# Kernel tuning notes

Hardware: AMD Instinct MI355X
Metric: run time of the kernel (lower is better)

## Reference

```python
import jax, jax.numpy as jnp
import numpy as np

N_NODES = 100000
N_EDGES = 1600000
D = 128


def _gine_layer(x, src, dst, e, W1, b1, W2, b2):
    # message: relu(x_j + e_ji), aggregate: sum at destination
    m = jax.nn.relu(x[src] + e)                       # [E, D]
    agg = jax.ops.segment_sum(m, dst, num_segments=x.shape[0])  # [N, D]
    h = agg + x                                       # (1 + eps) * x_i with eps = 0
    h = jax.nn.relu(jnp.dot(h, W1) + b1)
    return jnp.dot(h, W2) + b2


def setup_inputs() -> dict:
    key = jax.random.key(0)
    ks = jax.random.split(key, 16)
    s = 0.05
    inp = {
        "x": jax.random.normal(ks[0], (N_NODES, D), dtype=jnp.float32),
        "edge_index": jax.random.randint(ks[1], (2, N_EDGES), 0, N_NODES, dtype=jnp.int64) if jax.config.jax_enable_x64 else jax.random.randint(ks[1], (2, N_EDGES), 0, N_NODES, dtype=jnp.int32),
        "edge_attr": jax.random.randint(ks[2], (N_EDGES,), 0, 100, dtype=jnp.int32),
        "edge_emb": jax.random.normal(ks[3], (100, D), dtype=jnp.float32) * s,
        "Win": jax.random.normal(ks[4], (D, D), dtype=jnp.float32) * s,
        "b_in": jnp.zeros((D,), dtype=jnp.float32),
        "W1_0": jax.random.normal(ks[5], (D, D), dtype=jnp.float32) * s,
        "b1_0": jnp.zeros((D,), dtype=jnp.float32),
        "W2_0": jax.random.normal(ks[6], (D, D), dtype=jnp.float32) * s,
        "b2_0": jnp.zeros((D,), dtype=jnp.float32),
        "W1_1": jax.random.normal(ks[7], (D, D), dtype=jnp.float32) * s,
        "b1_1": jnp.zeros((D,), dtype=jnp.float32),
        "W2_1": jax.random.normal(ks[8], (D, D), dtype=jnp.float32) * s,
        "b2_1": jnp.zeros((D,), dtype=jnp.float32),
        "Wout": jax.random.normal(ks[9], (D, 1), dtype=jnp.float32) * s,
        "b_out": jnp.zeros((1,), dtype=jnp.float32),
    }
    return inp


def reference(x, edge_index, edge_attr, edge_emb, Win, b_in,
              W1_0, b1_0, W2_0, b2_0, W1_1, b1_1, W2_1, b2_1,
              Wout, b_out):
    src, dst = edge_index[0], edge_index[1]
    e = edge_emb[edge_attr]                 # [E, D] edge-attribute embedding lookup
    h = jnp.dot(x, Win) + b_in              # input_proj
    # layer 0: GINEConv + residual add + relu (norm=none, dropout off)
    h = jax.nn.relu(_gine_layer(h, src, dst, e, W1_0, b1_0, W2_0, b2_0) + h)
    # layer 1
    h = jax.nn.relu(_gine_layer(h, src, dst, e, W1_1, b1_1, W2_1, b2_1) + h)
    # output_mlp: single Linear(hidden, 1); no final activation, no pooling
    return jnp.dot(h, Wout) + b_out
```

## Files before the change

kernel.cpp:

```cpp
#include <hip/hip_runtime.h>

#define NN 100000
#define D 128
#define CHUNK 4096
#define BCSTRIDE 392
#define AGG_BLOCKS 1024

typedef __attribute__((ext_vector_type(8))) short short8;
typedef __attribute__((ext_vector_type(8))) unsigned short ushort8;
typedef __attribute__((ext_vector_type(4))) float f32x4;

__device__ __forceinline__ float4 ld4(const float* p) { return *(const float4*)p; }

__device__ __forceinline__ unsigned short f2bf(float f) {
    unsigned int u = __float_as_uint(f);
    unsigned int r = u + 0x7fffu + ((u >> 16) & 1u);
    return (unsigned short)(r >> 16);
}
__device__ __forceinline__ float bf2f(unsigned short h) {
    return __uint_as_float(((unsigned int)h) << 16);
}
__device__ __forceinline__ int swz(int rloc, int c) {
    return rloc * 128 + ((c + ((rloc >> 2) << 4)) & 127);
}

__global__ __launch_bounds__(256) void setup_all(
    const float* __restrict__ W0, const float* __restrict__ W1,
    const float* __restrict__ W2, const float* __restrict__ W3,
    const float* __restrict__ W4, unsigned short* __restrict__ wp,
    const float* __restrict__ emb, unsigned int* __restrict__ embp,
    int* __restrict__ binTotal)
{
    const int T = blockIdx.x * 256 + threadIdx.x;
    if (T < 5 * D * D) {
        const int w = T / (D * D);
        const int t = T % (D * D);
        const float* W = (w == 0) ? W0 : (w == 1) ? W1 : (w == 2) ? W2 : (w == 3) ? W3 : W4;
        const int j  = t & 7;
        const int L  = (t >> 3) & 63;
        const int ks = (t >> 9) & 3;
        const int nt = t >> 11;
        const float v = W[(ks * 32 + (L >> 4) * 8 + j) * D + nt * 16 + (L & 15)];
        const unsigned short h = f2bf(v);
        unsigned short* hi = wp + (size_t)w * 2 * D * D;
        hi[t] = h;
        hi[D * D + t] = f2bf(v - bf2f(h));
    } else if (T < 5 * D * D + 6400) {
        const int i = T - 5 * D * D;
        embp[i] = (unsigned int)f2bf(emb[i * 2]) | ((unsigned int)f2bf(emb[i * 2 + 1]) << 16);
    } else if (T < 5 * D * D + 6400 + BCSTRIDE) {
        binTotal[T - 5 * D * D - 6400] = 0;
    }
}

__global__ __launch_bounds__(256) void gemm_in(
    const float* __restrict__ A1,
    const unsigned short* __restrict__ Whi, const unsigned short* __restrict__ Wlo,
    const float* __restrict__ bias,
    unsigned short* __restrict__ out_hi, unsigned short* __restrict__ out_lo, int N)
{
    __shared__ __align__(16) unsigned int uT[64 * 128];
    const int t  = threadIdx.x;
    const int wv = t >> 6;
    const int L  = t & 63;
    const int lr = L & 15;
    const int q  = L >> 4;
    const int rbase = wv * 16;
    const int row = blockIdx.x * 64 + rbase + lr;

    short8 ahi[4], alo[4];
    #pragma unroll
    for (int ks = 0; ks < 4; ++ks) {
        float v[8];
        if (row < N) {
            const int off = row * D + ks * 32 + q * 8;
            const float4 x0 = ld4(&A1[off]), x1 = ld4(&A1[off + 4]);
            v[0] = x0.x; v[1] = x0.y; v[2] = x0.z; v[3] = x0.w;
            v[4] = x1.x; v[5] = x1.y; v[6] = x1.z; v[7] = x1.w;
        } else {
            #pragma unroll
            for (int j = 0; j < 8; ++j) v[j] = 0.f;
        }
        #pragma unroll
        for (int j = 0; j < 8; ++j) {
            const unsigned short h = f2bf(v[j]);
            ahi[ks][j] = (short)h;
            alo[ks][j] = (short)f2bf(v[j] - bf2f(h));
        }
    }

    f32x4 acc[8];
    #pragma unroll
    for (int nt = 0; nt < 8; ++nt) acc[nt] = (f32x4){0.f, 0.f, 0.f, 0.f};

    #pragma unroll
    for (int ks = 0; ks < 4; ++ks)
        #pragma unroll
        for (int nt = 0; nt < 8; ++nt) {
            const int base = ((nt * 4 + ks) * 64 + L) * 8;
            const short8 bhi = *(const short8*)&Whi[base];
            const short8 blo = *(const short8*)&Wlo[base];
            acc[nt] = __builtin_amdgcn_mfma_f32_16x16x32_bf16(alo[ks], bhi, acc[nt], 0, 0, 0);
            acc[nt] = __builtin_amdgcn_mfma_f32_16x16x32_bf16(ahi[ks], blo, acc[nt], 0, 0, 0);
            acc[nt] = __builtin_amdgcn_mfma_f32_16x16x32_bf16(ahi[ks], bhi, acc[nt], 0, 0, 0);
        }

    #pragma unroll
    for (int nt = 0; nt < 8; ++nt) {
        const float b = bias[nt * 16 + lr];
        #pragma unroll
        for (int r = 0; r < 4; ++r) {
            const int rloc = rbase + q * 4 + r;
            uT[swz(rloc, nt * 16 + lr)] = __float_as_uint(acc[nt][r] + b);
        }
    }
    __syncthreads();
    if (row < N) {
        const int rl = rbase + lr;
        #pragma unroll
        for (int ks = 0; ks < 4; ++ks) {
            const unsigned int* p = &uT[swz(rl, ks * 32 + q * 8)];
            const int off = row * D + ks * 32 + q * 8;
            ushort8 oh, ol;
            #pragma unroll
            for (int j = 0; j < 8; ++j) {
                const float o = __uint_as_float(p[j]);
                const unsigned short h = f2bf(o);
                oh[j] = h;
                ol[j] = f2bf(o - bf2f(h));
            }
            *(ushort8*)&out_hi[off] = oh;
            *(ushort8*)&out_lo[off] = ol;
        }
    }
}

template<bool LAST>
__global__ __launch_bounds__(256) void mlp_fused(
    const float* __restrict__ agg,
    const unsigned short* __restrict__ h_hi, const unsigned short* __restrict__ h_lo,
    const unsigned short* __restrict__ W1hi, const unsigned short* __restrict__ W1lo,
    const float* __restrict__ b1,
    const unsigned short* __restrict__ W2hi, const unsigned short* __restrict__ W2lo,
    const float* __restrict__ b2,
    unsigned short* __restrict__ out_hi, unsigned short* __restrict__ out_lo,
    const float* __restrict__ Wout, const float* __restrict__ bout,
    float* __restrict__ outv, int N)
{
    __shared__ __align__(16) unsigned int uT[64 * 128];
    const int t  = threadIdx.x;
    const int wv = t >> 6;
    const int L  = t & 63;
    const int lr = L & 15;
    const int q  = L >> 4;
    const int rbase = wv * 16;
    const int row = blockIdx.x * 64 + rbase + lr;
    const int rl = rbase + lr;

    ushort8 hh[4], ll[4];
    short8 ahi[4], alo[4];
    #pragma unroll
    for (int ks = 0; ks < 4; ++ks) {
        float v[8];
        if (row < N) {
            const int off = row * D + ks * 32 + q * 8;
            const float4 x0 = ld4(&agg[off]), x1 = ld4(&agg[off + 4]);
            hh[ks] = *(const ushort8*)&h_hi[off];
            ll[ks] = *(const ushort8*)&h_lo[off];
            v[0] = x0.x; v[1] = x0.y; v[2] = x0.z; v[3] = x0.w;
            v[4] = x1.x; v[5] = x1.y; v[6] = x1.z; v[7] = x1.w;
        } else {
            hh[ks] = (ushort8)0; ll[ks] = (ushort8)0;
            #pragma unroll
            for (int j = 0; j < 8; ++j) v[j] = 0.f;
        }
        #pragma unroll
        for (int j = 0; j < 8; ++j) {
            v[j] += bf2f(hh[ks][j]) + bf2f(ll[ks][j]);
            const unsigned short h = f2bf(v[j]);
            ahi[ks][j] = (short)h;
            alo[ks][j] = (short)f2bf(v[j] - bf2f(h));
        }
    }

    f32x4 acc[8];
    #pragma unroll
    for (int nt = 0; nt < 8; ++nt) acc[nt] = (f32x4){0.f, 0.f, 0.f, 0.f};

    #pragma unroll
    for (int ks = 0; ks < 4; ++ks)
        #pragma unroll
        for (int nt = 0; nt < 8; ++nt) {
            const int base = ((nt * 4 + ks) * 64 + L) * 8;
            const short8 bhi = *(const short8*)&W1hi[base];
            const short8 blo = *(const short8*)&W1lo[base];
            acc[nt] = __builtin_amdgcn_mfma_f32_16x16x32_bf16(alo[ks], bhi, acc[nt], 0, 0, 0);
            acc[nt] = __builtin_amdgcn_mfma_f32_16x16x32_bf16(ahi[ks], blo, acc[nt], 0, 0, 0);
            acc[nt] = __builtin_amdgcn_mfma_f32_16x16x32_bf16(ahi[ks], bhi, acc[nt], 0, 0, 0);
        }

    #pragma unroll
    for (int nt = 0; nt < 8; ++nt) {
        const float b = b1[nt * 16 + lr];
        #pragma unroll
        for (int r = 0; r < 4; ++r) {
            const int rloc = rbase + q * 4 + r;
            const float o = fmaxf(acc[nt][r] + b, 0.f);
            const unsigned int hi = f2bf(o);
            const unsigned int lo = f2bf(o - bf2f((unsigned short)hi));
            uT[swz(rloc, nt * 16 + lr)] = (hi << 16) | lo;
        }
    }
    __syncthreads();

    short8 uhi[4], ulo[4];
    #pragma unroll
    for (int ks = 0; ks < 4; ++ks) {
        const unsigned int* p = &uT[swz(rl, ks * 32 + q * 8)];
        #pragma unroll
        for (int j = 0; j < 8; ++j) {
            const unsigned int v = p[j];
            uhi[ks][j] = (short)(v >> 16);
            ulo[ks][j] = (short)(v & 0xffffu);
        }
    }

    f32x4 acc2[8];
    #pragma unroll
    for (int nt = 0; nt < 8; ++nt) acc2[nt] = (f32x4){0.f, 0.f, 0.f, 0.f};

    #pragma unroll
    for (int ks = 0; ks < 4; ++ks)
        #pragma unroll
        for (int nt = 0; nt < 8; ++nt) {
            const int base = ((nt * 4 + ks) * 64 + L) * 8;
            const short8 bhi = *(const short8*)&W2hi[base];
            const short8 blo = *(const short8*)&W2lo[base];
            acc2[nt] = __builtin_amdgcn_mfma_f32_16x16x32_bf16(ulo[ks], bhi, acc2[nt], 0, 0, 0);
            acc2[nt] = __builtin_amdgcn_mfma_f32_16x16x32_bf16(uhi[ks], blo, acc2[nt], 0, 0, 0);
            acc2[nt] = __builtin_amdgcn_mfma_f32_16x16x32_bf16(uhi[ks], bhi, acc2[nt], 0, 0, 0);
        }
    __syncthreads();

    #pragma unroll
    for (int nt = 0; nt < 8; ++nt) {
        const float b = b2[nt * 16 + lr];
        #pragma unroll
        for (int r = 0; r < 4; ++r) {
            const int rloc = rbase + q * 4 + r;
            uT[swz(rloc, nt * 16 + lr)] = __float_as_uint(acc2[nt][r] + b);
        }
    }
    __syncthreads();

    if (LAST) {
        float accv = 0.f;
        if (row < N) {
            #pragma unroll
            for (int ks = 0; ks < 4; ++ks) {
                const unsigned int* p = &uT[swz(rl, ks * 32 + q * 8)];
                const float4 w0 = ld4(&Wout[ks * 32 + q * 8]);
                const float4 w1 = ld4(&Wout[ks * 32 + q * 8 + 4]);
                float o[8];
                #pragma unroll
                for (int j = 0; j < 8; ++j)
                    o[j] = fmaxf(__uint_as_float(p[j]) + bf2f(hh[ks][j]) + bf2f(ll[ks][j]), 0.f);
                accv += o[0] * w0.x + o[1] * w0.y + o[2] * w0.z + o[3] * w0.w;
                accv += o[4] * w1.x + o[5] * w1.y + o[6] * w1.z + o[7] * w1.w;
            }
        }
        accv += __shfl_xor(accv, 16);
        accv += __shfl_xor(accv, 32);
        if (q == 0 && row < N) outv[row] = accv + bout[0];
    } else if (row < N) {
        #pragma unroll
        for (int ks = 0; ks < 4; ++ks) {
            const unsigned int* p = &uT[swz(rl, ks * 32 + q * 8)];
            const int off = row * D + ks * 32 + q * 8;
            ushort8 oh, ol;
            #pragma unroll
            for (int j = 0; j < 8; ++j) {
                const float o = fmaxf(__uint_as_float(p[j]) + bf2f(hh[ks][j]) + bf2f(ll[ks][j]), 0.f);
                const unsigned short h = f2bf(o);
                oh[j] = h;
                ol[j] = f2bf(o - bf2f(h));
            }
            *(ushort8*)&out_hi[off] = oh;
            *(ushort8*)&out_lo[off] = ol;
        }
    }
}

__global__ __launch_bounds__(256) void bin_count(
    const int* __restrict__ dst, int* __restrict__ blkcnt,
    int* __restrict__ binTotal, int E, int nbins)
{
    __shared__ int hist[512];
    const int t = threadIdx.x;
    const int i = blockIdx.x;
    for (int k = t; k < nbins; k += 256) hist[k] = 0;
    __syncthreads();
    const int e0 = i * CHUNK;
    const int e1 = min(E, e0 + CHUNK);
    for (int e = e0 + t; e < e1; e += 256) atomicAdd(&hist[dst[e] >> 8], 1);
    __syncthreads();
    for (int k = t; k < nbins; k += 256) {
        const int c = hist[k];
        blkcnt[i * BCSTRIDE + k] = c;
        if (c) atomicAdd(&binTotal[k], c);
    }
}

__global__ __launch_bounds__(512) void bin_scan(
    const int* __restrict__ binTotal, int* __restrict__ binStart,
    int* __restrict__ binCursor, int nbins)
{
    __shared__ int s[512];
    const int t = threadIdx.x;
    const int v = (t < nbins) ? binTotal[t] : 0;
    s[t] = v;
    __syncthreads();
    for (int off = 1; off < 512; off <<= 1) {
        const int x = (t >= off) ? s[t - off] : 0;
        __syncthreads();
        s[t] += x;
        __syncthreads();
    }
    if (t < nbins) { binStart[t] = s[t] - v; binCursor[t] = s[t] - v; }
    if (t == 0)    binStart[nbins] = s[511];
}

__global__ __launch_bounds__(256) void bin_scatter(
    const int* __restrict__ src, const int* __restrict__ dst,
    const int* __restrict__ attr, const int* __restrict__ blkcnt,
    int* __restrict__ binCursor, int2* __restrict__ binned, int E, int nbins)
{
    __shared__ int cur[512];
    const int t = threadIdx.x;
    const int i = blockIdx.x;
    for (int k = t; k < nbins; k += 256) {
        const int c = blkcnt[i * BCSTRIDE + k];
        if (c) cur[k] = atomicAdd(&binCursor[k], c);
    }
    __syncthreads();
    const int e0 = i * CHUNK;
    const int e1 = min(E, e0 + CHUNK);
    for (int e = e0 + t; e < e1; e += 256) {
        const int d = dst[e];
        const int p = atomicAdd(&cur[d >> 8], 1);
        binned[p] = make_int2(src[e] | (attr[e] << 20), d);
    }
}

__global__ __launch_bounds__(256) void bin_build(
    const int2* __restrict__ binned, const int* __restrict__ binStart,
    int* __restrict__ rowptr, int* __restrict__ epack, int N)
{
    __shared__ int hist[256];
    __shared__ int scn[256];
    __shared__ int curn[256];
    const int t = threadIdx.x;
    const int b = blockIdx.x;
    hist[t] = 0;
    __syncthreads();
    const int ebeg = binStart[b];
    const int eend = binStart[b + 1];
    for (int e = ebeg + t; e < eend; e += 256) atomicAdd(&hist[binned[e].y & 255], 1);
    __syncthreads();
    scn[t] = hist[t];
    __syncthreads();
    for (int off = 1; off < 256; off <<= 1) {
        const int x = (t >= off) ? scn[t - off] : 0;
        __syncthreads();
        scn[t] += x;
        __syncthreads();
    }
    const int node = b * 256 + t;
    if (node < N) rowptr[node] = ebeg + scn[t];
    curn[t] = ebeg + scn[t] - hist[t];
    __syncthreads();
    for (int e = ebeg + t; e < eend; e += 256) {
        const int2 v = binned[e];
        const int p = atomicAdd(&curn[v.y & 255], 1);
        epack[p] = v.x;
    }
}

__global__ __launch_bounds__(512) void aggregate(
    const unsigned int* __restrict__ hu,
    const int* __restrict__ rowptr, const int* __restrict__ epack,
    const unsigned int* __restrict__ embp, float* __restrict__ agg, int N)
{
    __shared__ unsigned int semb[100 * 64];
    const int t = threadIdx.x;
    for (int i = t; i < 100 * 64; i += 512) semb[i] = embp[i];
    __syncthreads();

    const int wv   = t >> 6;
    const int lane = t & 63;

    for (int node = blockIdx.x * 8 + wv; node < N; node += AGG_BLOCKS * 8) {
        int start = (node == 0) ? 0 : rowptr[node - 1];
        int end   = rowptr[node];
        start = __builtin_amdgcn_readfirstlane(start);
        end   = __builtin_amdgcn_readfirstlane(end);

        float ax = 0.f, ay = 0.f;
        int j = start;

        for (; j < end && (j & 3); ++j) {
            const int p0 = __builtin_amdgcn_readfirstlane(epack[j]);
            const unsigned int u0 = hu[(p0 & 0xFFFFF) * 64 + lane];
            const unsigned int v0 = semb[(p0 >> 20) * 64 + lane];
            ax += fmaxf(__uint_as_float(u0 << 16) + __uint_as_float(v0 << 16), 0.f);
            ay += fmaxf(__uint_as_float(u0 & 0xffff0000u) + __uint_as_float(v0 & 0xffff0000u), 0.f);
        }

        for (; j + 7 < end; j += 8) {
            const int4 pk0 = *(const int4*)&epack[j];
            const int4 pk1 = *(const int4*)&epack[j + 4];
            int p[8];
            p[0] = __builtin_amdgcn_readfirstlane(pk0.x);
            p[1] = __builtin_amdgcn_readfirstlane(pk0.y);
            p[2] = __builtin_amdgcn_readfirstlane(pk0.z);
            p[3] = __builtin_amdgcn_readfirstlane(pk0.w);
            p[4] = __builtin_amdgcn_readfirstlane(pk1.x);
            p[5] = __builtin_amdgcn_readfirstlane(pk1.y);
            p[6] = __builtin_amdgcn_readfirstlane(pk1.z);
            p[7] = __builtin_amdgcn_readfirstlane(pk1.w);
            unsigned int u[8], v[8];
            #pragma unroll
            for (int k = 0; k < 8; ++k) u[k] = hu[(p[k] & 0xFFFFF) * 64 + lane];
            #pragma unroll
            for (int k = 0; k < 8; ++k) v[k] = semb[(p[k] >> 20) * 64 + lane];
            #pragma unroll
            for (int k = 0; k < 8; ++k) {
                ax += fmaxf(__uint_as_float(u[k] << 16) + __uint_as_float(v[k] << 16), 0.f);
                ay += fmaxf(__uint_as_float(u[k] & 0xffff0000u) + __uint_as_float(v[k] & 0xffff0000u), 0.f);
            }
        }

        if (j + 3 < end) {
            const int4 pk0 = *(const int4*)&epack[j];
            int p[4];
            p[0] = __builtin_amdgcn_readfirstlane(pk0.x);
            p[1] = __builtin_amdgcn_readfirstlane(pk0.y);
            p[2] = __builtin_amdgcn_readfirstlane(pk0.z);
            p[3] = __builtin_amdgcn_readfirstlane(pk0.w);
            unsigned int u[4], v[4];
            #pragma unroll
            for (int k = 0; k < 4; ++k) u[k] = hu[(p[k] & 0xFFFFF) * 64 + lane];
            #pragma unroll
            for (int k = 0; k < 4; ++k) v[k] = semb[(p[k] >> 20) * 64 + lane];
            #pragma unroll
            for (int k = 0; k < 4; ++k) {
                ax += fmaxf(__uint_as_float(u[k] << 16) + __uint_as_float(v[k] << 16), 0.f);
                ay += fmaxf(__uint_as_float(u[k] & 0xffff0000u) + __uint_as_float(v[k] & 0xffff0000u), 0.f);
            }
            j += 4;
        }

        for (; j < end; ++j) {
            const int p0 = __builtin_amdgcn_readfirstlane(epack[j]);
            const unsigned int u0 = hu[(p0 & 0xFFFFF) * 64 + lane];
            const unsigned int v0 = semb[(p0 >> 20) * 64 + lane];
            ax += fmaxf(__uint_as_float(u0 << 16) + __uint_as_float(v0 << 16), 0.f);
            ay += fmaxf(__uint_as_float(u0 & 0xffff0000u) + __uint_as_float(v0 & 0xffff0000u), 0.f);
        }

        float2 o; o.x = ax; o.y = ay;
        ((float2*)agg)[node * 64 + lane] = o;
    }
}

extern "C" void kernel_launch(void* const* d_in, const int* in_sizes, int n_in,
                              void* d_out, int out_size, void* d_ws, size_t ws_size,
                              hipStream_t stream)
{
    const float* x     = (const float*)d_in[0];
    const int*   ei    = (const int*)  d_in[1];
    const int*   attr  = (const int*)  d_in[2];
    const float* emb   = (const float*)d_in[3];
    const float* Win   = (const float*)d_in[4];
    const float* b_in  = (const float*)d_in[5];
    const float* W1_0  = (const float*)d_in[6];
    const float* b1_0  = (const float*)d_in[7];
    const float* W2_0  = (const float*)d_in[8];
    const float* b2_0  = (const float*)d_in[9];
    const float* W1_1  = (const float*)d_in[10];
    const float* b1_1  = (const float*)d_in[11];
    const float* W2_1  = (const float*)d_in[12];
    const float* b2_1  = (const float*)d_in[13];
    const float* Wout  = (const float*)d_in[14];
    const float* b_out = (const float*)d_in[15];
    float* out = (float*)d_out;

    const int N = NN;
    const int E = in_sizes[2];
    const int* srcp = ei;
    const int* dstp = ei + E;
    const int nbins = (N + 255) >> 8;
    const int eblocks = (E + CHUNK - 1) / CHUNK;

    unsigned short* h_hi = (unsigned short*)d_ws;
    unsigned short* h_lo = h_hi + (size_t)N * D;
    float* agg    = (float*)(h_lo + (size_t)N * D);
    int*   rowptr = (int*)(agg + (size_t)N * D);
    int*   epack  = rowptr + N;
    unsigned short* wp = (unsigned short*)(epack + E);
    unsigned short* Whi[5], *Wlo[5];
    for (int i = 0; i < 5; ++i) {
        Whi[i] = wp + (size_t)i * 2 * D * D;
        Wlo[i] = Whi[i] + D * D;
    }
    unsigned int* embp = (unsigned int*)(wp + 5 * 2 * D * D);
    int2* binned    = (int2*)agg;
    int*  blkcnt    = (int*)(binned + E);
    int*  binTotal  = blkcnt + eblocks * BCSTRIDE;
    int*  binStart  = binTotal + BCSTRIDE;
    int*  binCursor = binStart + BCSTRIDE;

    dim3 blk(256);
    const int fgrid = (N + 63) / 64;
    const int sgrid = (5 * D * D + 6400 + BCSTRIDE + 255) / 256;

    setup_all<<<sgrid, blk, 0, stream>>>(Win, W1_0, W2_0, W1_1, W2_1, wp, emb, embp, binTotal);

    bin_count<<<eblocks, blk, 0, stream>>>(dstp, blkcnt, binTotal, E, nbins);
    bin_scan<<<1, 512, 0, stream>>>(binTotal, binStart, binCursor, nbins);
    bin_scatter<<<eblocks, blk, 0, stream>>>(srcp, dstp, attr, blkcnt, binCursor, binned, E, nbins);
    bin_build<<<nbins, blk, 0, stream>>>(binned, binStart, rowptr, epack, N);

    gemm_in<<<fgrid, blk, 0, stream>>>(x, Whi[0], Wlo[0], b_in, h_hi, h_lo, N);

    aggregate<<<AGG_BLOCKS, dim3(512), 0, stream>>>(
        (const unsigned int*)h_hi, rowptr, epack, embp, agg, N);
    mlp_fused<false><<<fgrid, blk, 0, stream>>>(
        agg, h_hi, h_lo, Whi[1], Wlo[1], b1_0, Whi[2], Wlo[2], b2_0,
        h_hi, h_lo, nullptr, nullptr, nullptr, N);

    aggregate<<<AGG_BLOCKS, dim3(512), 0, stream>>>(
        (const unsigned int*)h_hi, rowptr, epack, embp, agg, N);
    mlp_fused<true><<<fgrid, blk, 0, stream>>>(
        agg, h_hi, h_lo, Whi[3], Wlo[3], b1_1, Whi[4], Wlo[4], b2_1,
        nullptr, nullptr, Wout, b_out, out, N);
}
```

Baseline: 458.4 us.

## Process two 16-row groups per wave to reuse weight fragments in GEMM kernels

gemm_in and mlp_fused now give each wave 32 rows as two 16-row MFMA groups, so blocks cover 128 rows and the grid is halved. Each hi/lo weight fragment loaded from global memory now feeds MFMAs for both groups, which halves weight-load traffic per row. To offset the extra accumulator registers, the residual h_hi/h_lo values are reloaded from global memory in the epilogue instead of being held in registers. The same LDS staging buffer is reused for both groups one after the other. This raises register pressure and may lower occupancy, and it adds a second read of the residual activations.

```diff
diff --git a/kernel.cpp b/kernel.cpp
--- a/kernel.cpp
+++ b/kernel.cpp
@@ -66,32 +66,40 @@
     const int lr = L & 15;
     const int q  = L >> 4;
     const int rbase = wv * 16;
-    const int row = blockIdx.x * 64 + rbase + lr;
-
-    short8 ahi[4], alo[4];
-    #pragma unroll
-    for (int ks = 0; ks < 4; ++ks) {
-        float v[8];
-        if (row < N) {
-            const int off = row * D + ks * 32 + q * 8;
-            const float4 x0 = ld4(&A1[off]), x1 = ld4(&A1[off + 4]);
-            v[0] = x0.x; v[1] = x0.y; v[2] = x0.z; v[3] = x0.w;
-            v[4] = x1.x; v[5] = x1.y; v[6] = x1.z; v[7] = x1.w;
-        } else {
-            #pragma unroll
-            for (int j = 0; j < 8; ++j) v[j] = 0.f;
-        }
-        #pragma unroll
-        for (int j = 0; j < 8; ++j) {
-            const unsigned short h = f2bf(v[j]);
-            ahi[ks][j] = (short)h;
-            alo[ks][j] = (short)f2bf(v[j] - bf2f(h));
-        }
-    }
-
-    f32x4 acc[8];
-    #pragma unroll
-    for (int nt = 0; nt < 8; ++nt) acc[nt] = (f32x4){0.f, 0.f, 0.f, 0.f};
+    const int row0 = blockIdx.x * 128 + wv * 32 + lr;
+    const int rl = rbase + lr;
+
+    short8 ahi[2][4], alo[2][4];
+    #pragma unroll
+    for (int g = 0; g < 2; ++g) {
+        const int row = row0 + g * 16;
+        #pragma unroll
+        for (int ks = 0; ks < 4; ++ks) {
+            float v[8];
+            if (row < N) {
+                const int off = row * D + ks * 32 + q * 8;
+                const float4 x0 = ld4(&A1[off]), x1 = ld4(&A1[off + 4]);
+                v[0] = x0.x; v[1] = x0.y; v[2] = x0.z; v[3] = x0.w;
+                v[4] = x1.x; v[5] = x1.y; v[6] = x1.z; v[7] = x1.w;
+            } else {
+                #pragma unroll
+                for (int j = 0; j < 8; ++j) v[j] = 0.f;
+            }
+            #pragma unroll
+            for (int j = 0; j < 8; ++j) {
+                const unsigned short h = f2bf(v[j]);
+                ahi[g][ks][j] = (short)h;
+                alo[g][ks][j] = (short)f2bf(v[j] - bf2f(h));
+            }
+        }
+    }
+    __syncthreads();
+
+    f32x4 acc[2][8];
+    #pragma unroll
+    for (int g = 0; g < 2; ++g)
+        #pragma unroll
+        for (int nt = 0; nt < 8; ++nt) acc[g][nt] = (f32x4){0.f, 0.f, 0.f, 0.f};
 
     #pragma unroll
     for (int ks = 0; ks < 4; ++ks)
@@ -100,37 +108,43 @@
             const int base = ((nt * 4 + ks) * 64 + L) * 8;
             const short8 bhi = *(const short8*)&Whi[base];
             const short8 blo = *(const short8*)&Wlo[base];
-            acc[nt] = __builtin_amdgcn_mfma_f32_16x16x32_bf16(alo[ks], bhi, acc[nt], 0, 0, 0);
-            acc[nt] = __builtin_amdgcn_mfma_f32_16x16x32_bf16(ahi[ks], blo, acc[nt], 0, 0, 0);
-            acc[nt] = __builtin_amdgcn_mfma_f32_16x16x32_bf16(ahi[ks], bhi, acc[nt], 0, 0, 0);
-        }
-
-    #pragma unroll
-    for (int nt = 0; nt < 8; ++nt) {
-        const float b = bias[nt * 16 + lr];
-        #pragma unroll
-        for (int r = 0; r < 4; ++r) {
-            const int rloc = rbase + q * 4 + r;
-            uT[swz(rloc, nt * 16 + lr)] = __float_as_uint(acc[nt][r] + b);
-        }
-    }
-    __syncthreads();
-    if (row < N) {
-        const int rl = rbase + lr;
-        #pragma unroll
-        for (int ks = 0; ks < 4; ++ks) {
-            const unsigned int* p = &uT[swz(rl, ks * 32 + q * 8)];
-            const int off = row * D + ks * 32 + q * 8;
-            ushort8 oh, ol;
-            #pragma unroll
-            for (int j = 0; j < 8; ++j) {
-                const float o = __uint_as_float(p[j]);
-                const unsigned short h = f2bf(o);
-                oh[j] = h;
-                ol[j] = f2bf(o - bf2f(h));
-            }
-            *(ushort8*)&out_hi[off] = oh;
-            *(ushort8*)&out_lo[off] = ol;
+            acc[0][nt] = __builtin_amdgcn_mfma_f32_16x16x32_bf16(alo[0][ks], bhi, acc[0][nt], 0, 0, 0);
+            acc[0][nt] = __builtin_amdgcn_mfma_f32_16x16x32_bf16(ahi[0][ks], blo, acc[0][nt], 0, 0, 0);
+            acc[0][nt] = __builtin_amdgcn_mfma_f32_16x16x32_bf16(ahi[0][ks], bhi, acc[0][nt], 0, 0, 0);
+            acc[1][nt] = __builtin_amdgcn_mfma_f32_16x16x32_bf16(alo[1][ks], bhi, acc[1][nt], 0, 0, 0);
+            acc[1][nt] = __builtin_amdgcn_mfma_f32_16x16x32_bf16(ahi[1][ks], blo, acc[1][nt], 0, 0, 0);
+            acc[1][nt] = __builtin_amdgcn_mfma_f32_16x16x32_bf16(ahi[1][ks], bhi, acc[1][nt], 0, 0, 0);
+        }
+    __syncthreads();
+
+    #pragma unroll
+    for (int g = 0; g < 2; ++g) {
+        const int row = row0 + g * 16;
+        #pragma unroll
+        for (int nt = 0; nt < 8; ++nt) {
+            const float b = bias[nt * 16 + lr];
+            #pragma unroll
+            for (int r = 0; r < 4; ++r) {
+                const int rloc = rbase + q * 4 + r;
+                uT[swz(rloc, nt * 16 + lr)] = __float_as_uint(acc[g][nt][r] + b);
+            }
+        }
+        if (row < N) {
+            #pragma unroll
+            for (int ks = 0; ks < 4; ++ks) {
+                const unsigned int* p = &uT[swz(rl, ks * 32 + q * 8)];
+                const int off = row * D + ks * 32 + q * 8;
+                ushort8 oh, ol;
+                #pragma unroll
+                for (int j = 0; j < 8; ++j) {
+                    const float o = __uint_as_float(p[j]);
+                    const unsigned short h = f2bf(o);
+                    oh[j] = h;
+                    ol[j] = f2bf(o - bf2f(h));
+                }
+                *(ushort8*)&out_hi[off] = oh;
+                *(ushort8*)&out_lo[off] = ol;
+            }
         }
     }
 }
@@ -138,12 +152,12 @@
 template<bool LAST>
 __global__ __launch_bounds__(256) void mlp_fused(
     const float* __restrict__ agg,
-    const unsigned short* __restrict__ h_hi, const unsigned short* __restrict__ h_lo,
+    const unsigned short* h_hi, const unsigned short* h_lo,
     const unsigned short* __restrict__ W1hi, const unsigned short* __restrict__ W1lo,
     const float* __restrict__ b1,
     const unsigned short* __restrict__ W2hi, const unsigned short* __restrict__ W2lo,
     const float* __restrict__ b2,
-    unsigned short* __restrict__ out_hi, unsigned short* __restrict__ out_lo,
+    unsigned short* out_hi, unsigned short* out_lo,
     const float* __restrict__ Wout, const float* __restrict__ bout,
     float* __restrict__ outv, int N)
 {
@@ -154,38 +168,44 @@
     const int lr = L & 15;
     const int q  = L >> 4;
     const int rbase = wv * 16;
-    const int row = blockIdx.x * 64 + rbase + lr;
+    const int row0 = blockIdx.x * 128 + wv * 32 + lr;
     const int rl = rbase + lr;
 
-    ushort8 hh[4], ll[4];
-    short8 ahi[4], alo[4];
-    #pragma unroll
-    for (int ks = 0; ks < 4; ++ks) {
-        float v[8];
-        if (row < N) {
-            const int off = row * D + ks * 32 + q * 8;
-            const float4 x0 = ld4(&agg[off]), x1 = ld4(&agg[off + 4]);
-            hh[ks] = *(const ushort8*)&h_hi[off];
-            ll[ks] = *(const ushort8*)&h_lo[off];
-            v[0] = x0.x; v[1] = x0.y; v[2] = x0.z; v[3] = x0.w;
-            v[4] = x1.x; v[5] = x1.y; v[6] = x1.z; v[7] = x1.w;
-        } else {
-            hh[ks] = (ushort8)0; ll[ks] = (ushort8)0;
-            #pragma unroll
-            for (int j = 0; j < 8; ++j) v[j] = 0.f;
-        }
-        #pragma unroll
-        for (int j = 0; j < 8; ++j) {
-            v[j] += bf2f(hh[ks][j]) + bf2f(ll[ks][j]);
-            const unsigned short h = f2bf(v[j]);
-            ahi[ks][j] = (short)h;
-            alo[ks][j] = (short)f2bf(v[j] - bf2f(h));
-        }
-    }
-
-    f32x4 acc[8];
-    #pragma unroll
-    for (int nt = 0; nt < 8; ++nt) acc[nt] = (f32x4){0.f, 0.f, 0.f, 0.f};
+    short8 ahi[2][4], alo[2][4];
+    #pragma unroll
+    for (int g = 0; g < 2; ++g) {
+        const int row = row0 + g * 16;
+        #pragma unroll
+        for (int ks = 0; ks < 4; ++ks) {
+            float v[8];
+            if (row < N) {
+                const int off = row * D + ks * 32 + q * 8;
+                const float4 x0 = ld4(&agg[off]), x1 = ld4(&agg[off + 4]);
+                const ushort8 hh = *(const ushort8*)&h_hi[off];
+                const ushort8 ll = *(const ushort8*)&h_lo[off];
+                v[0] = x0.x; v[1] = x0.y; v[2] = x0.z; v[3] = x0.w;
+                v[4] = x1.x; v[5] = x1.y; v[6] = x1.z; v[7] = x1.w;
+                #pragma unroll
+                for (int j = 0; j < 8; ++j) v[j] += bf2f(hh[j]) + bf2f(ll[j]);
+            } else {
+                #pragma unroll
+                for (int j = 0; j < 8; ++j) v[j] = 0.f;
+            }
+            #pragma unroll
+            for (int j = 0; j < 8; ++j) {
+                const unsigned short h = f2bf(v[j]);
+                ahi[g][ks][j] = (short)h;
+                alo[g][ks][j] = (short)f2bf(v[j] - bf2f(h));
+            }
+        }
+    }
+    __syncthreads();
+
+    f32x4 acc[2][8];
+    #pragma unroll
+    for (int g = 0; g < 2; ++g)
+        #pragma unroll
+        for (int nt = 0; nt < 8; ++nt) acc[g][nt] = (f32x4){0.f, 0.f, 0.f, 0.f};
 
     #pragma unroll
     for (int ks = 0; ks < 4; ++ks)
@@ -194,40 +214,48 @@
             const int base = ((nt * 4 + ks) * 64 + L) * 8;
             const short8 bhi = *(const short8*)&W1hi[base];
             const short8 blo = *(const short8*)&W1lo[base];
-            acc[nt] = __builtin_amdgcn_mfma_f32_16x16x32_bf16(alo[ks], bhi, acc[nt], 0, 0, 0);
-            acc[nt] = __builtin_amdgcn_mfma_f32_16x16x32_bf16(ahi[ks], blo, acc[nt], 0, 0, 0);
-            acc[nt] = __builtin_amdgcn_mfma_f32_16x16x32_bf16(ahi[ks], bhi, acc[nt], 0, 0, 0);
-        }
-
-    #pragma unroll
-    for (int nt = 0; nt < 8; ++nt) {
-        const float b = b1[nt * 16 + lr];
-        #pragma unroll
-        for (int r = 0; r < 4; ++r) {
-            const int rloc = rbase + q * 4 + r;
-            const float o = fmaxf(acc[nt][r] + b, 0.f);
-            const unsigned int hi = f2bf(o);
-            const unsigned int lo = f2bf(o - bf2f((unsigned short)hi));
-            uT[swz(rloc, nt * 16 + lr)] = (hi << 16) | lo;
-        }
-    }
-    __syncthreads();
-
-    short8 uhi[4], ulo[4];
-    #pragma unroll
-    for (int ks = 0; ks < 4; ++ks) {
-        const unsigned int* p = &uT[swz(rl, ks * 32 + q * 8)];
-        #pragma unroll
-        for (int j = 0; j < 8; ++j) {
-            const unsigned int v = p[j];
-            uhi[ks][j] = (short)(v >> 16);
-            ulo[ks][j] = (short)(v & 0xffffu);
-        }
-    }
-
-    f32x4 acc2[8];
-    #pragma unroll
-    for (int nt = 0; nt < 8; ++nt) acc2[nt] = (f32x4){0.f, 0.f, 0.f, 0.f};
+            acc[0][nt] = __builtin_amdgcn_mfma_f32_16x16x32_bf16(alo[0][ks], bhi, acc[0][nt], 0, 0, 0);
+            acc[0][nt] = __builtin_amdgcn_mfma_f32_16x16x32_bf16(ahi[0][ks], blo, acc[0][nt], 0, 0, 0);
+            acc[0][nt] = __builtin_amdgcn_mfma_f32_16x16x32_bf16(ahi[0][ks], bhi, acc[0][nt], 0, 0, 0);
+            acc[1][nt] = __builtin_amdgcn_mfma_f32_16x16x32_bf16(alo[1][ks], bhi, acc[1][nt], 0, 0, 0);
+            acc[1][nt] = __builtin_amdgcn_mfma_f32_16x16x32_bf16(ahi[1][ks], blo, acc[1][nt], 0, 0, 0);
+            acc[1][nt] = __builtin_amdgcn_mfma_f32_16x16x32_bf16(ahi[1][ks], bhi, acc[1][nt], 0, 0, 0);
+        }
+    __syncthreads();
+
+    short8 uhi[2][4], ulo[2][4];
+    #pragma unroll
+    for (int g = 0; g < 2; ++g) {
+        #pragma unroll
+        for (int nt = 0; nt < 8; ++nt) {
+            const float b = b1[nt * 16 + lr];
+            #pragma unroll
+            for (int r = 0; r < 4; ++r) {
+                const int rloc = rbase + q * 4 + r;
+                const float o = fmaxf(acc[g][nt][r] + b, 0.f);
+                const unsigned int hi = f2bf(o);
+                const unsigned int lo = f2bf(o - bf2f((unsigned short)hi));
+                uT[swz(rloc, nt * 16 + lr)] = (hi << 16) | lo;
+            }
+        }
+        #pragma unroll
+        for (int ks = 0; ks < 4; ++ks) {
+            const unsigned int* p = &uT[swz(rl, ks * 32 + q * 8)];
+            #pragma unroll
+            for (int j = 0; j < 8; ++j) {
+                const unsigned int v = p[j];
+                uhi[g][ks][j] = (short)(v >> 16);
+                ulo[g][ks][j] = (short)(v & 0xffffu);
+            }
+        }
+    }
+    __syncthreads();
+
+    f32x4 acc2[2][8];
+    #pragma unroll
+    for (int g = 0; g < 2; ++g)
+        #pragma unroll
+        for (int nt = 0; nt < 8; ++nt) acc2[g][nt] = (f32x4){0.f, 0.f, 0.f, 0.f};
 
     #pragma unroll
     for (int ks = 0; ks < 4; ++ks)
@@ -236,57 +264,67 @@
             const int base = ((nt * 4 + ks) * 64 + L) * 8;
             const short8 bhi = *(const short8*)&W2hi[base];
             const short8 blo = *(const short8*)&W2lo[base];
-            acc2[nt] = __builtin_amdgcn_mfma_f32_16x16x32_bf16(ulo[ks], bhi, acc2[nt], 0, 0, 0);
-            acc2[nt] = __builtin_amdgcn_mfma_f32_16x16x32_bf16(uhi[ks], blo, acc2[nt], 0, 0, 0);
-            acc2[nt] = __builtin_amdgcn_mfma_f32_16x16x32_bf16(uhi[ks], bhi, acc2[nt], 0, 0, 0);
-        }
-    __syncthreads();
-
-    #pragma unroll
-    for (int nt = 0; nt < 8; ++nt) {
-        const float b = b2[nt * 16 + lr];
-        #pragma unroll
-        for (int r = 0; r < 4; ++r) {
-            const int rloc = rbase + q * 4 + r;
-            uT[swz(rloc, nt * 16 + lr)] = __float_as_uint(acc2[nt][r] + b);
-        }
-    }
-    __syncthreads();
-
-    if (LAST) {
-        float accv = 0.f;
-        if (row < N) {
+            acc2[0][nt] = __builtin_amdgcn_mfma_f32_16x16x32_bf16(ulo[0][ks], bhi, acc2[0][nt], 0, 0, 0);
+            acc2[0][nt] = __builtin_amdgcn_mfma_f32_16x16x32_bf16(uhi[0][ks], blo, acc2[0][nt], 0, 0, 0);
+            acc2[0][nt] = __builtin_amdgcn_mfma_f32_16x16x32_bf16(uhi[0][ks], bhi, acc2[0][nt], 0, 0, 0);
+            acc2[1][nt] = __builtin_amdgcn_mfma_f32_16x16x32_bf16(ulo[1][ks], bhi, acc2[1][nt], 0, 0, 0);
+            acc2[1][nt] = __builtin_amdgcn_mfma_f32_16x16x32_bf16(uhi[1][ks], blo, acc2[1][nt], 0, 0, 0);
+            acc2[1][nt] = __builtin_amdgcn_mfma_f32_16x16x32_bf16(uhi[1][ks], bhi, acc2[1][nt], 0, 0, 0);
+        }
+    __syncthreads();
+
+    #pragma unroll
+    for (int g = 0; g < 2; ++g) {
+        const int row = row0 + g * 16;
+        #pragma unroll
+        for (int nt = 0; nt < 8; ++nt) {
+            const float b = b2[nt * 16 + lr];
+            #pragma unroll
+            for (int r = 0; r < 4; ++r) {
+                const int rloc = rbase + q * 4 + r;
+                uT[swz(rloc, nt * 16 + lr)] = __float_as_uint(acc2[g][nt][r] + b);
+            }
+        }
+        if (LAST) {
+            float accv = 0.f;
+            if (row < N) {
+                #pragma unroll
+                for (int ks = 0; ks < 4; ++ks) {
+                    const unsigned int* p = &uT[swz(rl, ks * 32 + q * 8)];
+                    const int off = row * D + ks * 32 + q * 8;
+                    const ushort8 hh = *(const ushort8*)&h_hi[off];
+                    const ushort8 ll = *(const ushort8*)&h_lo[off];
+                    const float4 w0 = ld4(&Wout[ks * 32 + q * 8]);
+                    const float4 w1 = ld4(&Wout[ks * 32 + q * 8 + 4]);
+                    float o[8];
+                    #pragma unroll
+                    for (int j = 0; j < 8; ++j)
+                        o[j] = fmaxf(__uint_as_float(p[j]) + bf2f(hh[j]) + bf2f(ll[j]), 0.f);
+                    accv += o[0] * w0.x + o[1] * w0.y + o[2] * w0.z + o[3] * w0.w;
+                    accv += o[4] * w1.x + o[5] * w1.y + o[6] * w1.z + o[7] * w1.w;
+                }
+            }
+            accv += __shfl_xor(accv, 16);
+            accv += __shfl_xor(accv, 32);
+            if (q == 0 && row < N) outv[row] = accv + bout[0];
+        } else if (row < N) {
             #pragma unroll
             for (int ks = 0; ks < 4; ++ks) {
                 const unsigned int* p = &uT[swz(rl, ks * 32 + q * 8)];
-                const float4 w0 = ld4(&Wout[ks * 32 + q * 8]);
-                const float4 w1 = ld4(&Wout[ks * 32 + q * 8 + 4]);
-                float o[8];
+                const int off = row * D + ks * 32 + q * 8;
+                const ushort8 hh = *(const ushort8*)&h_hi[off];
+                const ushort8 ll = *(const ushort8*)&h_lo[off];
+                ushort8 oh, ol;
                 #pragma unroll
-                for (int j = 0; j < 8; ++j)
-                    o[j] = fmaxf(__uint_as_float(p[j]) + bf2f(hh[ks][j]) + bf2f(ll[ks][j]), 0.f);
-                accv += o[0] * w0.x + o[1] * w0.y + o[2] * w0.z + o[3] * w0.w;
-                accv += o[4] * w1.x + o[5] * w1.y + o[6] * w1.z + o[7] * w1.w;
-            }
-        }
-        accv += __shfl_xor(accv, 16);
-        accv += __shfl_xor(accv, 32);
-        if (q == 0 && row < N) outv[row] = accv + bout[0];
-    } else if (row < N) {
-        #pragma unroll
-        for (int ks = 0; ks < 4; ++ks) {
-            const unsigned int* p = &uT[swz(rl, ks * 32 + q * 8)];
-            const int off = row * D + ks * 32 + q * 8;
-            ushort8 oh, ol;
-            #pragma unroll
-            for (int j = 0; j < 8; ++j) {
-                const float o = fmaxf(__uint_as_float(p[j]) + bf2f(hh[ks][j]) + bf2f(ll[ks][j]), 0.f);
-                const unsigned short h = f2bf(o);
-                oh[j] = h;
-                ol[j] = f2bf(o - bf2f(h));
-            }
-            *(ushort8*)&out_hi[off] = oh;
-            *(ushort8*)&out_lo[off] = ol;
+                for (int j = 0; j < 8; ++j) {
+                    const float o = fmaxf(__uint_as_float(p[j]) + bf2f(hh[j]) + bf2f(ll[j]), 0.f);
+                    const unsigned short h = f2bf(o);
+                    oh[j] = h;
+                    ol[j] = f2bf(o - bf2f(h));
+                }
+                *(ushort8*)&out_hi[off] = oh;
+                *(ushort8*)&out_lo[off] = ol;
+            }
         }
     }
 }
@@ -521,7 +559,7 @@
     int*  binCursor = binStart + BCSTRIDE;
 
     dim3 blk(256);
-    const int fgrid = (N + 63) / 64;
+    const int fgrid = (N + 127) / 128;
     const int sgrid = (5 * D * D + 6400 + BCSTRIDE + 255) / 256;
 
     setup_all<<<sgrid, blk, 0, stream>>>(Win, W1_0, W2_0, W1_1, W2_1, wp, emb, embp, binTotal);
```

Measured after the change: 483.3 us. 5.4% more time.

## Share A tile through LDS so each wave computes all rows for two column tiles

Applied to the files above, without the earlier changes.

The dense GEMM kernels (input projection and fused MLP) now stage the split-bf16 A tile in LDS and have each wave compute all 64 rows for its own 2 of the 8 column tiles. Before, each wave handled 16 rows against all 8 column tiles. Each wave now reads a quarter of the weight fragments from global/L2, cutting redundant weight traffic and the live weight registers. The residual h_hi/h_lo values are reloaded from global memory in the epilogue instead of being held in registers, which lowers register pressure. The cost is extra LDS traffic and barriers, plus dropping __restrict__ on those pointers.

```diff
diff --git a/kernel.cpp b/kernel.cpp
--- a/kernel.cpp
+++ b/kernel.cpp
@@ -22,6 +22,42 @@
 }
 __device__ __forceinline__ int swz(int rloc, int c) {
     return rloc * 128 + ((c + ((rloc >> 2) << 4)) & 127);
+}
+
+__device__ __forceinline__ void coop_gemm(
+    const unsigned int* uT,
+    const unsigned short* __restrict__ Whi, const unsigned short* __restrict__ Wlo,
+    int wv, int L, int lr, int q, f32x4 acc[4][2])
+{
+    #pragma unroll
+    for (int ks = 0; ks < 4; ++ks) {
+        short8 ahi[4], alo[4];
+        #pragma unroll
+        for (int m = 0; m < 4; ++m) {
+            const unsigned int* p = &uT[swz(m * 16 + lr, ks * 32 + q * 8)];
+            const uint4 a0 = *(const uint4*)p;
+            const uint4 a1 = *(const uint4*)(p + 4);
+            const unsigned int w[8] = {a0.x, a0.y, a0.z, a0.w, a1.x, a1.y, a1.z, a1.w};
+            #pragma unroll
+            for (int j = 0; j < 8; ++j) {
+                ahi[m][j] = (short)(w[j] >> 16);
+                alo[m][j] = (short)(w[j] & 0xffffu);
+            }
+        }
+        #pragma unroll
+        for (int n = 0; n < 2; ++n) {
+            const int nt = wv * 2 + n;
+            const int base = ((nt * 4 + ks) * 64 + L) * 8;
+            const short8 bhi = *(const short8*)&Whi[base];
+            const short8 blo = *(const short8*)&Wlo[base];
+            #pragma unroll
+            for (int m = 0; m < 4; ++m) {
+                acc[m][n] = __builtin_amdgcn_mfma_f32_16x16x32_bf16(alo[m], bhi, acc[m][n], 0, 0, 0);
+                acc[m][n] = __builtin_amdgcn_mfma_f32_16x16x32_bf16(ahi[m], blo, acc[m][n], 0, 0, 0);
+                acc[m][n] = __builtin_amdgcn_mfma_f32_16x16x32_bf16(ahi[m], bhi, acc[m][n], 0, 0, 0);
+            }
+        }
+    }
 }
 
 __global__ __launch_bounds__(256) void setup_all(
@@ -67,8 +103,8 @@
     const int q  = L >> 4;
     const int rbase = wv * 16;
     const int row = blockIdx.x * 64 + rbase + lr;
-
-    short8 ahi[4], alo[4];
+    const int rl  = rbase + lr;
+
     #pragma unroll
     for (int ks = 0; ks < 4; ++ks) {
         float v[8];
@@ -81,42 +117,39 @@
             #pragma unroll
             for (int j = 0; j < 8; ++j) v[j] = 0.f;
         }
+        unsigned int pk[8];
         #pragma unroll
         for (int j = 0; j < 8; ++j) {
-            const unsigned short h = f2bf(v[j]);
-            ahi[ks][j] = (short)h;
-            alo[ks][j] = (short)f2bf(v[j] - bf2f(h));
-        }
-    }
-
-    f32x4 acc[8];
-    #pragma unroll
-    for (int nt = 0; nt < 8; ++nt) acc[nt] = (f32x4){0.f, 0.f, 0.f, 0.f};
-
-    #pragma unroll
-    for (int ks = 0; ks < 4; ++ks)
-        #pragma unroll
-        for (int nt = 0; nt < 8; ++nt) {
-            const int base = ((nt * 4 + ks) * 64 + L) * 8;
-            const short8 bhi = *(const short8*)&Whi[base];
-            const short8 blo = *(const short8*)&Wlo[base];
-            acc[nt] = __builtin_amdgcn_mfma_f32_16x16x32_bf16(alo[ks], bhi, acc[nt], 0, 0, 0);
-            acc[nt] = __builtin_amdgcn_mfma_f32_16x16x32_bf16(ahi[ks], blo, acc[nt], 0, 0, 0);
-            acc[nt] = __builtin_amdgcn_mfma_f32_16x16x32_bf16(ahi[ks], bhi, acc[nt], 0, 0, 0);
-        }
-
-    #pragma unroll
-    for (int nt = 0; nt < 8; ++nt) {
+            const unsigned int hi = f2bf(v[j]);
+            pk[j] = (hi << 16) | f2bf(v[j] - bf2f((unsigned short)hi));
+        }
+        unsigned int* p = &uT[swz(rl, ks * 32 + q * 8)];
+        *(uint4*)p       = make_uint4(pk[0], pk[1], pk[2], pk[3]);
+        *(uint4*)(p + 4) = make_uint4(pk[4], pk[5], pk[6], pk[7]);
+    }
+    __syncthreads();
+
+    f32x4 acc[4][2];
+    #pragma unroll
+    for (int m = 0; m < 4; ++m)
+        #pragma unroll
+        for (int n = 0; n < 2; ++n) acc[m][n] = (f32x4){0.f, 0.f, 0.f, 0.f};
+    coop_gemm(uT, Whi, Wlo, wv, L, lr, q, acc);
+    __syncthreads();
+
+    #pragma unroll
+    for (int n = 0; n < 2; ++n) {
+        const int nt = wv * 2 + n;
         const float b = bias[nt * 16 + lr];
         #pragma unroll
-        for (int r = 0; r < 4; ++r) {
-            const int rloc = rbase + q * 4 + r;
-            uT[swz(rloc, nt * 16 + lr)] = __float_as_uint(acc[nt][r] + b);
-        }
-    }
-    __syncthreads();
+        for (int m = 0; m < 4; ++m)
+            #pragma unroll
+            for (int r = 0; r < 4; ++r)
+                uT[swz(m * 16 + q * 4 + r, nt * 16 + lr)] = __float_as_uint(acc[m][n][r] + b);
+    }
+    __syncthreads();
+
     if (row < N) {
-        const int rl = rbase + lr;
         #pragma unroll
         for (int ks = 0; ks < 4; ++ks) {
             const unsigned int* p = &uT[swz(rl, ks * 32 + q * 8)];
@@ -138,12 +171,12 @@
 template<bool LAST>
 __global__ __launch_bounds__(256) void mlp_fused(
     const float* __restrict__ agg,
-    const unsigned short* __restrict__ h_hi, const unsigned short* __restrict__ h_lo,
+    const unsigned short* h_hi, const unsigned short* h_lo,
     const unsigned short* __restrict__ W1hi, const unsigned short* __restrict__ W1lo,
     const float* __restrict__ b1,
     const unsigned short* __restrict__ W2hi, const unsigned short* __restrict__ W2lo,
     const float* __restrict__ b2,
-    unsigned short* __restrict__ out_hi, unsigned short* __restrict__ out_lo,
+    unsigned short* out_hi, unsigned short* out_lo,
     const float* __restrict__ Wout, const float* __restrict__ bout,
     float* __restrict__ outv, int N)
 {
@@ -155,101 +188,77 @@
     const int q  = L >> 4;
     const int rbase = wv * 16;
     const int row = blockIdx.x * 64 + rbase + lr;
-    const int rl = rbase + lr;
-
-    ushort8 hh[4], ll[4];
-    short8 ahi[4], alo[4];
+    const int rl  = rbase + lr;
+
     #pragma unroll
     for (int ks = 0; ks < 4; ++ks) {
         float v[8];
         if (row < N) {
             const int off = row * D + ks * 32 + q * 8;
             const float4 x0 = ld4(&agg[off]), x1 = ld4(&agg[off + 4]);
-            hh[ks] = *(const ushort8*)&h_hi[off];
-            ll[ks] = *(const ushort8*)&h_lo[off];
+            const ushort8 hh = *(const ushort8*)&h_hi[off];
+            const ushort8 ll = *(const ushort8*)&h_lo[off];
             v[0] = x0.x; v[1] = x0.y; v[2] = x0.z; v[3] = x0.w;
             v[4] = x1.x; v[5] = x1.y; v[6] = x1.z; v[7] = x1.w;
+            #pragma unroll
+            for (int j = 0; j < 8; ++j) v[j] += bf2f(hh[j]) + bf2f(ll[j]);
         } else {
-            hh[ks] = (ushort8)0; ll[ks] = (ushort8)0;
             #pragma unroll
             for (int j = 0; j < 8; ++j) v[j] = 0.f;
         }
+        unsigned int pk[8];
         #pragma unroll
         for (int j = 0; j < 8; ++j) {
-            v[j] += bf2f(hh[ks][j]) + bf2f(ll[ks][j]);
-            const unsigned short h = f2bf(v[j]);
-            ahi[ks][j] = (short)h;
-            alo[ks][j] = (short)f2bf(v[j] - bf2f(h));
-        }
-    }
-
-    f32x4 acc[8];
-    #pragma unroll
-    for (int nt = 0; nt < 8; ++nt) acc[nt] = (f32x4){0.f, 0.f, 0.f, 0.f};
-
-    #pragma unroll
-    for (int ks = 0; ks < 4; ++ks)
-        #pragma unroll
-        for (int nt = 0; nt < 8; ++nt) {
-            const int base = ((nt * 4 + ks) * 64 + L) * 8;
-            const short8 bhi = *(const short8*)&W1hi[base];
-            const short8 blo = *(const short8*)&W1lo[base];
-            acc[nt] = __builtin_amdgcn_mfma_f32_16x16x32_bf16(alo[ks], bhi, acc[nt], 0, 0, 0);
-            acc[nt] = __builtin_amdgcn_mfma_f32_16x16x32_bf16(ahi[ks], blo, acc[nt], 0, 0, 0);
-            acc[nt] = __builtin_amdgcn_mfma_f32_16x16x32_bf16(ahi[ks], bhi, acc[nt], 0, 0, 0);
-        }
-
-    #pragma unroll
-    for (int nt = 0; nt < 8; ++nt) {
+            const unsigned int hi = f2bf(v[j]);
+            pk[j] = (hi << 16) | f2bf(v[j] - bf2f((unsigned short)hi));
+        }
+        unsigned int* p = &uT[swz(rl, ks * 32 + q * 8)];
+        *(uint4*)p       = make_uint4(pk[0], pk[1], pk[2], pk[3]);
+        *(uint4*)(p + 4) = make_uint4(pk[4], pk[5], pk[6], pk[7]);
+    }
+    __syncthreads();
+
+    f32x4 acc[4][2];
+    #pragma unroll
+    for (int m = 0; m < 4; ++m)
+        #pragma unroll
+        for (int n = 0; n < 2; ++n) acc[m][n] = (f32x4){0.f, 0.f, 0.f, 0.f};
+    coop_gemm(uT, W1hi, W1lo, wv, L, lr, q, acc);
+    __syncthreads();
+
+    #pragma unroll
+    for (int n = 0; n < 2; ++n) {
+        const int nt = wv * 2 + n;
         const float b = b1[nt * 16 + lr];
         #pragma unroll
-        for (int r = 0; r < 4; ++r) {
-            const int rloc = rbase + q * 4 + r;
-            const float o = fmaxf(acc[nt][r] + b, 0.f);
-            const unsigned int hi = f2bf(o);
-            const unsigned int lo = f2bf(o - bf2f((unsigned short)hi));
-            uT[swz(rloc, nt * 16 + lr)] = (hi << 16) | lo;
-        }
-    }
-    __syncthreads();
-
-    short8 uhi[4], ulo[4];
-    #pragma unroll
-    for (int ks = 0; ks < 4; ++ks) {
-        const unsigned int* p = &uT[swz(rl, ks * 32 + q * 8)];
-        #pragma unroll
-        for (int j = 0; j < 8; ++j) {
-            const unsigned int v = p[j];
-            uhi[ks][j] = (short)(v >> 16);
-            ulo[ks][j] = (short)(v & 0xffffu);
-        }
-    }
-
-    f32x4 acc2[8];
-    #pragma unroll
-    for (int nt = 0; nt < 8; ++nt) acc2[nt] = (f32x4){0.f, 0.f, 0.f, 0.f};
-
-    #pragma unroll
-    for (int ks = 0; ks < 4; ++ks)
-        #pragma unroll
-        for (int nt = 0; nt < 8; ++nt) {
-            const int base = ((nt * 4 + ks) * 64 + L) * 8;
-            const short8 bhi = *(const short8*)&W2hi[base];
-            const short8 blo = *(const short8*)&W2lo[base];
-            acc2[nt] = __builtin_amdgcn_mfma_f32_16x16x32_bf16(ulo[ks], bhi, acc2[nt], 0, 0, 0);
-            acc2[nt] = __builtin_amdgcn_mfma_f32_16x16x32_bf16(uhi[ks], blo, acc2[nt], 0, 0, 0);
-            acc2[nt] = __builtin_amdgcn_mfma_f32_16x16x32_bf16(uhi[ks], bhi, acc2[nt], 0, 0, 0);
-        }
-    __syncthreads();
-
-    #pragma unroll
-    for (int nt = 0; nt < 8; ++nt) {
+        for (int m = 0; m < 4; ++m)
+            #pragma unroll
+            for (int r = 0; r < 4; ++r) {
+                const float o = fmaxf(acc[m][n][r] + b, 0.f);
+                const unsigned int hi = f2bf(o);
+                const unsigned int lo = f2bf(o - bf2f((unsigned short)hi));
+                uT[swz(m * 16 + q * 4 + r, nt * 16 + lr)] = (hi << 16) | lo;
+            }
+    }
+    __syncthreads();
+
+    f32x4 acc2[4][2];
+    #pragma unroll
+    for (int m = 0; m < 4; ++m)
+        #pragma unroll
+        for (int n = 0; n < 2; ++n) acc2[m][n] = (f32x4){0.f, 0.f, 0.f, 0.f};
+    coop_gemm(uT, W2hi, W2lo, wv, L, lr, q, acc2);
+    __syncthreads();
+
+    #pragma unroll
+    for (int n = 0; n < 2; ++n) {
+        const int nt = wv * 2 + n;
         const float b = b2[nt * 16 + lr];
         #pragma unroll
-        for (int r = 0; r < 4; ++r) {
-            const int rloc = rbase + q * 4 + r;
-            uT[swz(rloc, nt * 16 + lr)] = __float_as_uint(acc2[nt][r] + b);
-        }
+        for (int m = 0; m < 4; ++m)
+            #pragma unroll
+            for (int r = 0; r < 4; ++r)
+                uT[swz(m * 16 + q * 4 + r, nt * 16 + lr)] = __float_as_uint(acc2[m][n][r] + b);
     }
     __syncthreads();
 
@@ -259,12 +268,15 @@
             #pragma unroll
             for (int ks = 0; ks < 4; ++ks) {
                 const unsigned int* p = &uT[swz(rl, ks * 32 + q * 8)];
+                const int off = row * D + ks * 32 + q * 8;
+                const ushort8 hh = *(const ushort8*)&h_hi[off];
+                const ushort8 ll = *(const ushort8*)&h_lo[off];
                 const float4 w0 = ld4(&Wout[ks * 32 + q * 8]);
                 const float4 w1 = ld4(&Wout[ks * 32 + q * 8 + 4]);
                 float o[8];
                 #pragma unroll
                 for (int j = 0; j < 8; ++j)
-                    o[j] = fmaxf(__uint_as_float(p[j]) + bf2f(hh[ks][j]) + bf2f(ll[ks][j]), 0.f);
+                    o[j] = fmaxf(__uint_as_float(p[j]) + bf2f(hh[j]) + bf2f(ll[j]), 0.f);
                 accv += o[0] * w0.x + o[1] * w0.y + o[2] * w0.z + o[3] * w0.w;
                 accv += o[4] * w1.x + o[5] * w1.y + o[6] * w1.z + o[7] * w1.w;
             }
@@ -277,10 +289,12 @@
         for (int ks = 0; ks < 4; ++ks) {
             const unsigned int* p = &uT[swz(rl, ks * 32 + q * 8)];
             const int off = row * D + ks * 32 + q * 8;
+            const ushort8 hh = *(const ushort8*)&h_hi[off];
+            const ushort8 ll = *(const ushort8*)&h_lo[off];
             ushort8 oh, ol;
             #pragma unroll
             for (int j = 0; j < 8; ++j) {
-                const float o = fmaxf(__uint_as_float(p[j]) + bf2f(hh[ks][j]) + bf2f(ll[ks][j]), 0.f);
+                const float o = fmaxf(__uint_as_float(p[j]) + bf2f(hh[j]) + bf2f(ll[j]), 0.f);
                 const unsigned short h = f2bf(o);
                 oh[j] = h;
                 ol[j] = f2bf(o - bf2f(h));
```

Measured after the change: 431.1 us. -5.9%, faster.
